# Kernel tuning notes

Measured on AMD Instinct MI355X. Metric: run time of the kernel, lower is better.

Reference implementation:

```python
import jax, jax.numpy as jnp
import numpy as np
import math

D_MODEL = 1024
N_HEADS = 16
D_HEAD = D_MODEL // N_HEADS


def setup_inputs() -> dict:
    key = jax.random.key(0)
    ks = jax.random.split(key, 5)
    B, T, C = 4, 2048, D_MODEL
    s = 1.0 / math.sqrt(C)
    return {
        "x": jax.random.normal(ks[0], (B, T, C), dtype=jnp.float32),
        "qkv_w": jax.random.normal(ks[1], (3 * C, C), dtype=jnp.float32) * s,
        "qkv_b": jnp.zeros((3 * C,), dtype=jnp.float32),
        "out_w": jax.random.normal(ks[2], (C, C), dtype=jnp.float32) * s,
        "out_b": jnp.zeros((C,), dtype=jnp.float32),
    }


def reference(x, qkv_w, qkv_b, out_w, out_b):
    B, T, C = x.shape
    H, Dh = N_HEADS, D_HEAD
    qkv = x @ qkv_w.T + qkv_b              # [B,T,3C] (torch Linear: x W^T + b)
    q, k, v = jnp.split(qkv, 3, axis=-1)
    # [B,T,C] -> [B,H,T,Dh]
    q = q.reshape(B, T, H, Dh).transpose(0, 2, 1, 3)
    k = k.reshape(B, T, H, Dh).transpose(0, 2, 1, 3)
    v = v.reshape(B, T, H, Dh).transpose(0, 2, 1, 3)
    att = jnp.einsum("bhqd,bhkd->bhqk", q, k) / math.sqrt(Dh)
    causal = jnp.tril(jnp.ones((T, T), dtype=bool))  # True = keep
    att = jnp.where(causal, att, -jnp.inf)
    att = jax.nn.softmax(att, axis=-1)
    y = jnp.einsum("bhqk,bhkd->bhqd", att, v)
    y = y.transpose(0, 2, 1, 3).reshape(B, T, C)
    return y @ out_w.T + out_b
```

## Files before the change

### kernel.cpp

```cpp
#include <hip/hip_runtime.h>

typedef __attribute__((ext_vector_type(4))) float f32x4;
typedef __attribute__((ext_vector_type(16))) float f32x16;
typedef __attribute__((ext_vector_type(8))) __bf16 bf16x8;
typedef __attribute__((ext_vector_type(4))) __bf16 bf16x4;
typedef __attribute__((ext_vector_type(2))) unsigned u32x2;

#define MFMA_B16(a,b,c) __builtin_amdgcn_mfma_f32_16x16x32_bf16((a),(b),(c),0,0,0)
#define MFMA32(a,b,c)  __builtin_amdgcn_mfma_f32_32x32x16_bf16((a),(b),(c),0,0,0)

static constexpr int T_LEN  = 2048;
static constexpr int C_DIM  = 1024;
static constexpr int H_NUM  = 16;
static constexpr int D_HEADc = 64;
static constexpr float Q_PRESCALE = 0.125f * 1.4426950408889634f;

__device__ __forceinline__ void async16(const void* g, void* l) {
  __builtin_amdgcn_global_load_lds(
      (const __attribute__((address_space(1))) unsigned int*)g,
      (__attribute__((address_space(3))) unsigned int*)l, 16, 0, 0);
}

__device__ __forceinline__ unsigned cvtpk(float lo, float hi) {
  unsigned r;
  asm("v_cvt_pk_bf16_f32 %0, %1, %2" : "=v"(r) : "v"(lo), "v"(hi));
  return r;
}

__global__ __launch_bounds__(256) void cvt3_kernel(const float* __restrict__ a, __bf16* __restrict__ da, int na,
                                                   const float* __restrict__ b, __bf16* __restrict__ db, int nb,
                                                   const float* __restrict__ c, __bf16* __restrict__ dc, int nc) {
  int i = blockIdx.x * 256 + threadIdx.x;
  const float* s;
  __bf16* d;
  long j;
  if (i < na) { s = a; d = da; j = i; }
  else if (i < na + nb) { s = b; d = db; j = i - na; }
  else if (i < na + nb + nc) { s = c; d = dc; j = i - na - nb; }
  else return;
  float4 f = reinterpret_cast<const float4*>(s)[j];
  bf16x4 o;
  o.x = (__bf16)f.x; o.y = (__bf16)f.y; o.z = (__bf16)f.z; o.w = (__bf16)f.w;
  reinterpret_cast<bf16x4*>(d)[j] = o;
}

__global__ __launch_bounds__(256) void gemm_qkv(const __bf16* __restrict__ A,
                                                const __bf16* __restrict__ W,
                                                const float* __restrict__ bias,
                                                __bf16* __restrict__ qb,
                                                __bf16* __restrict__ kb,
                                                __bf16* __restrict__ vb) {
  constexpr int K = 1024;
  __shared__ __bf16 As[128 * 64];
  __shared__ __bf16 Bs[128 * 64];
  const int tid = threadIdx.x;
  const int wid = tid >> 6, lane = tid & 63, l16 = lane & 15, lg = lane >> 4;
  const int r8 = lane >> 3, sl = lane & 7;
  const int r7 = l16 & 7;
  const int wm = wid >> 1, wn = wid & 1;
  const int m0 = blockIdx.x * 128, n0 = blockIdx.y * 128;

  f32x4 acc[4][4];
#pragma unroll
  for (int i = 0; i < 4; ++i)
#pragma unroll
    for (int j = 0; j < 4; ++j) acc[i][j] = f32x4{0.f, 0.f, 0.f, 0.f};

  for (int k0 = 0; k0 < K; k0 += 64) {
    __builtin_amdgcn_s_barrier();
#pragma unroll
    for (int it = 0; it < 4; ++it) {
      int chunk = it * 4 + wid;
      int row = chunk * 8 + r8;
      int scol = ((sl ^ (row & 7)) << 3);
      async16(A + (long)(m0 + row) * K + k0 + scol, &As[chunk * 512]);
      async16(W + (long)(n0 + row) * K + k0 + scol, &Bs[chunk * 512]);
    }
    asm volatile("s_waitcnt vmcnt(0)" ::: "memory");
    __builtin_amdgcn_s_barrier();
#pragma unroll
    for (int kt = 0; kt < 2; ++kt) {
      const int sw = ((((kt << 2) | lg) ^ r7) << 3);
      bf16x8 af[4], bfv[4];
#pragma unroll
      for (int mi = 0; mi < 4; ++mi)
        af[mi] = *reinterpret_cast<const bf16x8*>(&As[(wm * 64 + mi * 16 + l16) * 64 + sw]);
#pragma unroll
      for (int nt = 0; nt < 4; ++nt)
        bfv[nt] = *reinterpret_cast<const bf16x8*>(&Bs[(wn * 64 + nt * 16 + l16) * 64 + sw]);
#pragma unroll
      for (int mi = 0; mi < 4; ++mi)
#pragma unroll
        for (int nt = 0; nt < 4; ++nt)
          acc[mi][nt] = MFMA_B16(af[mi], bfv[nt], acc[mi][nt]);
    }
  }
#pragma unroll
  for (int mi = 0; mi < 4; ++mi)
#pragma unroll
    for (int nt = 0; nt < 4; ++nt)
#pragma unroll
      for (int r = 0; r < 4; ++r) {
        int m = m0 + wm * 64 + mi * 16 + lg * 4 + r;
        int n = n0 + wn * 64 + nt * 16 + l16;
        float val = acc[mi][nt][r] + bias[n];
        int which = n >> 10;
        int cc = n & 1023;
        int h = cc >> 6, d = cc & 63;
        long b = m >> 11;
        long t = m & 2047;
        if (which == 0) {
          qb[(((b * H_NUM + h) * T_LEN) + t) * D_HEADc + d] = (__bf16)(val * Q_PRESCALE);
        } else if (which == 1) {
          kb[(((b * H_NUM + h) * T_LEN) + t) * D_HEADc + d] = (__bf16)val;
        } else {
          vb[(((b * H_NUM + h) * D_HEADc) + d) * T_LEN + t] = (__bf16)val;
        }
      }
}

__global__ __launch_bounds__(256) void attn_kernel(const __bf16* __restrict__ q,
                                                   const __bf16* __restrict__ k,
                                                   const __bf16* __restrict__ vt,
                                                   __bf16* __restrict__ y) {
  __shared__ __bf16 Ks[2][64 * 64];
  __shared__ __bf16 Vs[2][64 * 64];
  const int tid = threadIdx.x;
  const int wid = tid >> 6, lane = tid & 63;
  const int l31 = lane & 31, hi = lane >> 5;
  const int r8 = lane >> 3, sl = lane & 7;
  const int r7 = l31 & 7;
  const int bid = blockIdx.x;
  const int pair = bid >> 6;
  const int bh = bid & 63;
  const __bf16* qg = q + (long)bh * T_LEN * D_HEADc;
  const __bf16* kg = k + (long)bh * T_LEN * D_HEADc;
  const __bf16* vg = vt + (long)bh * T_LEN * D_HEADc;
  const long bb = bh >> 4;
  const int h = bh & 15;

  union { unsigned short us[8]; bf16x8 v; } ones_u;
#pragma unroll
  for (int i = 0; i < 8; ++i) ones_u.us[i] = 0x3F80;
  const bf16x8 ones = ones_u.v;

  f32x16 z16;
#pragma unroll
  for (int r = 0; r < 16; ++r) z16[r] = 0.f;

  auto stage = [&](int buf, int t) {
    const int k0s = t * 64;
#pragma unroll
    for (int it = 0; it < 2; ++it) {
      int chunk = it * 4 + wid;
      int row = chunk * 8 + r8;
      int scol = ((sl ^ (row & 7)) << 3);
      async16(kg + (long)(k0s + row) * D_HEADc + scol, &Ks[buf][chunk * 512]);
      async16(vg + (long)row * T_LEN + k0s + scol, &Vs[buf][chunk * 512]);
    }
  };

  auto m3 = [](float a, float b, float c) { return fmaxf(fmaxf(a, b), c); };

  for (int ph = 0; ph < 2; ++ph) {
    const int qt = ph ? (15 - pair) : pair;
    const int q0 = qt * 128;
    const int qw = q0 + wid * 32;
    const int qglob = qw + l31;

    bf16x8 qf[4];
#pragma unroll
    for (int dt = 0; dt < 4; ++dt)
      qf[dt] = *reinterpret_cast<const bf16x8*>(qg + (long)qglob * D_HEADc + dt * 16 + hi * 8);

    f32x16 o[2];
    o[0] = z16; o[1] = z16;
    f32x16 lacc = z16;
    float m = -3e38f;

    const int ntiles = qt * 2 + 2;
    stage(0, 0);
    int cur = 0;
    for (int t = 0; t < ntiles; ++t) {
      if (t + 1 < ntiles) {
        stage(cur ^ 1, t + 1);
        asm volatile("s_waitcnt vmcnt(4)" ::: "memory");
      } else {
        asm volatile("s_waitcnt vmcnt(0)" ::: "memory");
      }
      __builtin_amdgcn_s_barrier();
      const int k0 = t * 64;
      if (k0 < qw + 32) {
        f32x16 s[2];
        __builtin_amdgcn_s_setprio(1);
        {
          const int swz = (hi ^ r7) << 3;
          bf16x8 kf0 = *reinterpret_cast<const bf16x8*>(&Ks[cur][l31 * 64 + swz]);
          bf16x8 kf1 = *reinterpret_cast<const bf16x8*>(&Ks[cur][(32 + l31) * 64 + swz]);
          s[0] = MFMA32(kf0, qf[0], z16);
          s[1] = MFMA32(kf1, qf[0], z16);
        }
#pragma unroll
        for (int dt = 1; dt < 4; ++dt) {
          const int swz = (((dt << 1) | hi) ^ r7) << 3;
          bf16x8 kf0 = *reinterpret_cast<const bf16x8*>(&Ks[cur][l31 * 64 + swz]);
          bf16x8 kf1 = *reinterpret_cast<const bf16x8*>(&Ks[cur][(32 + l31) * 64 + swz]);
          s[0] = MFMA32(kf0, qf[dt], s[0]);
          s[1] = MFMA32(kf1, qf[dt], s[1]);
        }
        __builtin_amdgcn_s_setprio(0);

        if (k0 + 63 > qw) {
#pragma unroll
          for (int r = 0; r < 16; ++r) {
            const int kb = (r & 3) + 8 * (r >> 2) + 4 * hi;
            if (k0 + kb > qglob) s[0][r] = -3e38f;
            if (k0 + 32 + kb > qglob) s[1][r] = -3e38f;
          }
        }

        float xv[11];
#pragma unroll
        for (int g = 0; g < 5; ++g) xv[g] = m3(s[0][3 * g], s[0][3 * g + 1], s[0][3 * g + 2]);
        xv[5] = m3(s[0][15], s[1][0], s[1][1]);
#pragma unroll
        for (int g = 0; g < 4; ++g) xv[6 + g] = m3(s[1][2 + 3 * g], s[1][3 + 3 * g], s[1][4 + 3 * g]);
        xv[10] = fmaxf(s[1][14], s[1][15]);
        float w0 = m3(xv[0], xv[1], xv[2]), w1 = m3(xv[3], xv[4], xv[5]);
        float w2 = m3(xv[6], xv[7], xv[8]), w3 = fmaxf(xv[9], xv[10]);
        float mx = fmaxf(m3(w0, w1, w2), w3);
        mx = fmaxf(mx, __shfl_xor(mx, 32));

        if (!__all(mx <= m + 8.f)) {
          const float mn = fmaxf(m, mx);
          const float al = exp2f(m - mn);
          m = mn;
          lacc[0] *= al;
#pragma unroll
          for (int di = 0; di < 2; ++di)
#pragma unroll
            for (int r = 0; r < 16; ++r) o[di][r] *= al;
        }
#pragma unroll
        for (int ki = 0; ki < 2; ++ki)
#pragma unroll
          for (int r = 0; r < 16; ++r) s[ki][r] = exp2f(s[ki][r] - m);

        unsigned pb[4][4];
#pragma unroll
        for (int ki = 0; ki < 2; ++ki) {
          unsigned d0 = cvtpk(s[ki][0], s[ki][1]),   d1 = cvtpk(s[ki][2], s[ki][3]);
          unsigned d2 = cvtpk(s[ki][4], s[ki][5]),   d3 = cvtpk(s[ki][6], s[ki][7]);
          unsigned d4 = cvtpk(s[ki][8], s[ki][9]),   d5 = cvtpk(s[ki][10], s[ki][11]);
          unsigned d6 = cvtpk(s[ki][12], s[ki][13]), d7 = cvtpk(s[ki][14], s[ki][15]);
          u32x2 a2 = __builtin_amdgcn_permlane32_swap(d0, d2, false, false);
          u32x2 b2 = __builtin_amdgcn_permlane32_swap(d1, d3, false, false);
          pb[ki * 2][0] = a2[0]; pb[ki * 2][1] = b2[0];
          pb[ki * 2][2] = a2[1]; pb[ki * 2][3] = b2[1];
          u32x2 c2 = __builtin_amdgcn_permlane32_swap(d4, d6, false, false);
          u32x2 e2 = __builtin_amdgcn_permlane32_swap(d5, d7, false, false);
          pb[ki * 2 + 1][0] = c2[0]; pb[ki * 2 + 1][1] = e2[0];
          pb[ki * 2 + 1][2] = c2[1]; pb[ki * 2 + 1][3] = e2[1];
        }

        __builtin_amdgcn_s_setprio(1);
#pragma unroll
        for (int kt = 0; kt < 4; ++kt) {
          union { unsigned u[4]; bf16x8 v; } pu;
#pragma unroll
          for (int w = 0; w < 4; ++w) pu.u[w] = pb[kt][w];
          const int swz = (((kt << 1) | hi) ^ r7) << 3;
          bf16x8 vf0 = *reinterpret_cast<const bf16x8*>(&Vs[cur][l31 * 64 + swz]);
          bf16x8 vf1 = *reinterpret_cast<const bf16x8*>(&Vs[cur][(32 + l31) * 64 + swz]);
          o[0] = MFMA32(vf0, pu.v, o[0]);
          o[1] = MFMA32(vf1, pu.v, o[1]);
          lacc = MFMA32(ones, pu.v, lacc);
        }
        __builtin_amdgcn_s_setprio(0);
      }
      __builtin_amdgcn_s_barrier();
      cur ^= 1;
    }

    const float inv = 1.f / lacc[0];
    const long row = bb * T_LEN + qglob;
#pragma unroll
    for (int di = 0; di < 2; ++di)
#pragma unroll
      for (int rr = 0; rr < 4; ++rr) {
        bf16x4 pk;
#pragma unroll
        for (int c = 0; c < 4; ++c) pk[c] = (__bf16)(o[di][rr * 4 + c] * inv);
        *reinterpret_cast<bf16x4*>(
            &y[row * C_DIM + h * D_HEADc + di * 32 + rr * 8 + hi * 4]) = pk;
      }
  }
}

__global__ __launch_bounds__(256) void gemm_proj(const __bf16* __restrict__ A,
                                                 const __bf16* __restrict__ W,
                                                 const float* __restrict__ bias,
                                                 float* __restrict__ out) {
  constexpr int K = 1024;
  __shared__ __bf16 As[128 * 64];
  __shared__ __bf16 Bs[128 * 64];
  const int tid = threadIdx.x;
  const int wid = tid >> 6, lane = tid & 63, l16 = lane & 15, lg = lane >> 4;
  const int r8 = lane >> 3, sl = lane & 7;
  const int r7 = l16 & 7;
  const int wm = wid >> 1, wn = wid & 1;
  const int m0 = blockIdx.x * 128, n0 = blockIdx.y * 128;

  f32x4 acc[4][4];
#pragma unroll
  for (int i = 0; i < 4; ++i)
#pragma unroll
    for (int j = 0; j < 4; ++j) acc[i][j] = f32x4{0.f, 0.f, 0.f, 0.f};

  for (int k0 = 0; k0 < K; k0 += 64) {
    __builtin_amdgcn_s_barrier();
#pragma unroll
    for (int it = 0; it < 4; ++it) {
      int chunk = it * 4 + wid;
      int row = chunk * 8 + r8;
      int scol = ((sl ^ (row & 7)) << 3);
      async16(A + (long)(m0 + row) * K + k0 + scol, &As[chunk * 512]);
      async16(W + (long)(n0 + row) * K + k0 + scol, &Bs[chunk * 512]);
    }
    asm volatile("s_waitcnt vmcnt(0)" ::: "memory");
    __builtin_amdgcn_s_barrier();
#pragma unroll
    for (int kt = 0; kt < 2; ++kt) {
      const int sw = ((((kt << 2) | lg) ^ r7) << 3);
      bf16x8 af[4], bfv[4];
#pragma unroll
      for (int mi = 0; mi < 4; ++mi)
        af[mi] = *reinterpret_cast<const bf16x8*>(&As[(wm * 64 + mi * 16 + l16) * 64 + sw]);
#pragma unroll
      for (int nt = 0; nt < 4; ++nt)
        bfv[nt] = *reinterpret_cast<const bf16x8*>(&Bs[(wn * 64 + nt * 16 + l16) * 64 + sw]);
#pragma unroll
      for (int mi = 0; mi < 4; ++mi)
#pragma unroll
        for (int nt = 0; nt < 4; ++nt)
          acc[mi][nt] = MFMA_B16(af[mi], bfv[nt], acc[mi][nt]);
    }
  }
#pragma unroll
  for (int mi = 0; mi < 4; ++mi)
#pragma unroll
    for (int nt = 0; nt < 4; ++nt)
#pragma unroll
      for (int r = 0; r < 4; ++r) {
        long m = m0 + wm * 64 + mi * 16 + lg * 4 + r;
        int n = n0 + wn * 64 + nt * 16 + l16;
        out[m * C_DIM + n] = acc[mi][nt][r] + bias[n];
      }
}

extern "C" void kernel_launch(void* const* d_in, const int* in_sizes, int n_in,
                              void* d_out, int out_size, void* d_ws, size_t ws_size,
                              hipStream_t stream) {
  const float* x     = (const float*)d_in[0];
  const float* qkv_w = (const float*)d_in[1];
  const float* qkv_b = (const float*)d_in[2];
  const float* out_w = (const float*)d_in[3];
  const float* out_b = (const float*)d_in[4];
  float* out = (float*)d_out;

  const long NX  = 8192L * 1024;
  const long NWQ = 3072L * 1024;
  const long NWO = 1024L * 1024;
  const size_t need = (size_t)(5 * NX + NWQ + NWO) * 2;
  if (ws_size < need) return;

  __bf16* xb   = (__bf16*)d_ws;
  __bf16* wqkv = xb + NX;
  __bf16* wout = wqkv + NWQ;
  __bf16* qb   = wout + NWO;
  __bf16* kb   = qb + NX;
  __bf16* vb   = kb + NX;
  __bf16* yb   = vb + NX;

  const int na = (int)(NX / 4), nb = (int)(NWQ / 4), nc = (int)(NWO / 4);
  cvt3_kernel<<<(na + nb + nc + 255) / 256, 256, 0, stream>>>(x, xb, na, qkv_w, wqkv, nb, out_w, wout, nc);

  gemm_qkv<<<dim3(64, 24), 256, 0, stream>>>(xb, wqkv, qkv_b, qb, kb, vb);
  attn_kernel<<<dim3(512), 256, 0, stream>>>(qb, kb, vb, yb);
  gemm_proj<<<dim3(64, 8), 256, 0, stream>>>(yb, wout, out_b, out);
}
```

Measured before the change: 199.3 us.

## Split attention KV loop across two wave groups with LDS merge

The attention kernel now runs 512 threads per block, one query tile per block, with two groups of four waves. Each group processes alternating 64-key tiles, and the groups' partial outputs and softmax stats are merged through LDS at the end. The old scheme, where each block paired two query tiles to balance causal work, is replaced by 1024 independent blocks ordered longest-first. This raises parallelism and shortens the per-block serial KV loop, at the cost of doubled LDS buffers, an extra merge step and possible idle waves on the odd last tile.

```diff
diff --git a/kernel.cpp b/kernel.cpp
--- a/kernel.cpp
+++ b/kernel.cpp
@@ -119,20 +119,25 @@
       }
 }
 
-__global__ __launch_bounds__(256) void attn_kernel(const __bf16* __restrict__ q,
-                                                   const __bf16* __restrict__ k,
-                                                   const __bf16* __restrict__ vt,
-                                                   __bf16* __restrict__ y) {
-  __shared__ __bf16 Ks[2][64 * 64];
-  __shared__ __bf16 Vs[2][64 * 64];
+__global__ __launch_bounds__(512, 4) void attn_kernel(const __bf16* __restrict__ q,
+                                                      const __bf16* __restrict__ k,
+                                                      const __bf16* __restrict__ vt,
+                                                      __bf16* __restrict__ y) {
+  __shared__ __bf16 Ks[2][2][64 * 64];
+  __shared__ __bf16 Vs[2][2][64 * 64];
   const int tid = threadIdx.x;
   const int wid = tid >> 6, lane = tid & 63;
   const int l31 = lane & 31, hi = lane >> 5;
   const int r8 = lane >> 3, sl = lane & 7;
   const int r7 = l31 & 7;
   const int bid = blockIdx.x;
-  const int pair = bid >> 6;
+  const int qt = 15 - (bid >> 6);
   const int bh = bid & 63;
+  const int grp = wid >> 2;
+  const int wq = wid & 3;
+  const int q0 = qt * 128;
+  const int qw = q0 + wq * 32;
+  const int qglob = qw + l31;
   const __bf16* qg = q + (long)bh * T_LEN * D_HEADc;
   const __bf16* kg = k + (long)bh * T_LEN * D_HEADc;
   const __bf16* vg = vt + (long)bh * T_LEN * D_HEADc;
@@ -148,141 +153,163 @@
 #pragma unroll
   for (int r = 0; r < 16; ++r) z16[r] = 0.f;
 
-  auto stage = [&](int buf, int t) {
-    const int k0s = t * 64;
-#pragma unroll
-    for (int it = 0; it < 2; ++it) {
-      int chunk = it * 4 + wid;
-      int row = chunk * 8 + r8;
+  bf16x8 qf[4];
+#pragma unroll
+  for (int dt = 0; dt < 4; ++dt)
+    qf[dt] = *reinterpret_cast<const bf16x8*>(qg + (long)qglob * D_HEADc + dt * 16 + hi * 8);
+
+  f32x16 o[2];
+  o[0] = z16; o[1] = z16;
+  f32x16 lacc = z16;
+  float m = -3e38f;
+
+  auto stage = [&](int buf, int i) {
+#pragma unroll
+    for (int it = 0; it < 4; ++it) {
+      int slot = it * 8 + wid;
+      int g = slot & 7;
+      int kind = slot >> 3;
+      int par = kind >> 1, isv = kind & 1;
+      int row = g * 8 + r8;
       int scol = ((sl ^ (row & 7)) << 3);
-      async16(kg + (long)(k0s + row) * D_HEADc + scol, &Ks[buf][chunk * 512]);
-      async16(vg + (long)row * T_LEN + k0s + scol, &Vs[buf][chunk * 512]);
+      int k0s = (2 * i + par) * 64;
+      if (!isv)
+        async16(kg + (long)(k0s + row) * D_HEADc + scol, &Ks[buf][par][g * 512]);
+      else
+        async16(vg + (long)row * T_LEN + k0s + scol, &Vs[buf][par][g * 512]);
     }
   };
 
   auto m3 = [](float a, float b, float c) { return fmaxf(fmaxf(a, b), c); };
 
-  for (int ph = 0; ph < 2; ++ph) {
-    const int qt = ph ? (15 - pair) : pair;
-    const int q0 = qt * 128;
-    const int qw = q0 + wid * 32;
-    const int qglob = qw + l31;
-
-    bf16x8 qf[4];
-#pragma unroll
-    for (int dt = 0; dt < 4; ++dt)
-      qf[dt] = *reinterpret_cast<const bf16x8*>(qg + (long)qglob * D_HEADc + dt * 16 + hi * 8);
-
-    f32x16 o[2];
-    o[0] = z16; o[1] = z16;
-    f32x16 lacc = z16;
-    float m = -3e38f;
-
-    const int ntiles = qt * 2 + 2;
-    stage(0, 0);
-    int cur = 0;
-    for (int t = 0; t < ntiles; ++t) {
-      if (t + 1 < ntiles) {
-        stage(cur ^ 1, t + 1);
-        asm volatile("s_waitcnt vmcnt(4)" ::: "memory");
-      } else {
-        asm volatile("s_waitcnt vmcnt(0)" ::: "memory");
-      }
-      __builtin_amdgcn_s_barrier();
-      const int k0 = t * 64;
-      if (k0 < qw + 32) {
-        f32x16 s[2];
-        __builtin_amdgcn_s_setprio(1);
-        {
-          const int swz = (hi ^ r7) << 3;
-          bf16x8 kf0 = *reinterpret_cast<const bf16x8*>(&Ks[cur][l31 * 64 + swz]);
-          bf16x8 kf1 = *reinterpret_cast<const bf16x8*>(&Ks[cur][(32 + l31) * 64 + swz]);
-          s[0] = MFMA32(kf0, qf[0], z16);
-          s[1] = MFMA32(kf1, qf[0], z16);
+  const int iters = qt + 1;
+  stage(0, 0);
+  int cur = 0;
+  for (int i = 0; i < iters; ++i) {
+    if (i + 1 < iters) {
+      stage(cur ^ 1, i + 1);
+      asm volatile("s_waitcnt vmcnt(4)" ::: "memory");
+    } else {
+      asm volatile("s_waitcnt vmcnt(0)" ::: "memory");
+    }
+    __builtin_amdgcn_s_barrier();
+    const int k0 = (2 * i + grp) * 64;
+    if (k0 < qw + 32) {
+      const __bf16* Kc = Ks[cur][grp];
+      const __bf16* Vc = Vs[cur][grp];
+      f32x16 s[2];
+      __builtin_amdgcn_s_setprio(1);
+      {
+        const int swz = (hi ^ r7) << 3;
+        bf16x8 kf0 = *reinterpret_cast<const bf16x8*>(&Kc[l31 * 64 + swz]);
+        bf16x8 kf1 = *reinterpret_cast<const bf16x8*>(&Kc[(32 + l31) * 64 + swz]);
+        s[0] = MFMA32(kf0, qf[0], z16);
+        s[1] = MFMA32(kf1, qf[0], z16);
+      }
+#pragma unroll
+      for (int dt = 1; dt < 4; ++dt) {
+        const int swz = (((dt << 1) | hi) ^ r7) << 3;
+        bf16x8 kf0 = *reinterpret_cast<const bf16x8*>(&Kc[l31 * 64 + swz]);
+        bf16x8 kf1 = *reinterpret_cast<const bf16x8*>(&Kc[(32 + l31) * 64 + swz]);
+        s[0] = MFMA32(kf0, qf[dt], s[0]);
+        s[1] = MFMA32(kf1, qf[dt], s[1]);
+      }
+      __builtin_amdgcn_s_setprio(0);
+
+      if (k0 + 63 > qw) {
+#pragma unroll
+        for (int r = 0; r < 16; ++r) {
+          const int kb = (r & 3) + 8 * (r >> 2) + 4 * hi;
+          if (k0 + kb > qglob) s[0][r] = -3e38f;
+          if (k0 + 32 + kb > qglob) s[1][r] = -3e38f;
         }
-#pragma unroll
-        for (int dt = 1; dt < 4; ++dt) {
-          const int swz = (((dt << 1) | hi) ^ r7) << 3;
-          bf16x8 kf0 = *reinterpret_cast<const bf16x8*>(&Ks[cur][l31 * 64 + swz]);
-          bf16x8 kf1 = *reinterpret_cast<const bf16x8*>(&Ks[cur][(32 + l31) * 64 + swz]);
-          s[0] = MFMA32(kf0, qf[dt], s[0]);
-          s[1] = MFMA32(kf1, qf[dt], s[1]);
-        }
-        __builtin_amdgcn_s_setprio(0);
-
-        if (k0 + 63 > qw) {
-#pragma unroll
-          for (int r = 0; r < 16; ++r) {
-            const int kb = (r & 3) + 8 * (r >> 2) + 4 * hi;
-            if (k0 + kb > qglob) s[0][r] = -3e38f;
-            if (k0 + 32 + kb > qglob) s[1][r] = -3e38f;
-          }
-        }
-
-        float xv[11];
-#pragma unroll
-        for (int g = 0; g < 5; ++g) xv[g] = m3(s[0][3 * g], s[0][3 * g + 1], s[0][3 * g + 2]);
-        xv[5] = m3(s[0][15], s[1][0], s[1][1]);
-#pragma unroll
-        for (int g = 0; g < 4; ++g) xv[6 + g] = m3(s[1][2 + 3 * g], s[1][3 + 3 * g], s[1][4 + 3 * g]);
-        xv[10] = fmaxf(s[1][14], s[1][15]);
-        float w0 = m3(xv[0], xv[1], xv[2]), w1 = m3(xv[3], xv[4], xv[5]);
-        float w2 = m3(xv[6], xv[7], xv[8]), w3 = fmaxf(xv[9], xv[10]);
-        float mx = fmaxf(m3(w0, w1, w2), w3);
-        mx = fmaxf(mx, __shfl_xor(mx, 32));
-
-        if (!__all(mx <= m + 8.f)) {
-          const float mn = fmaxf(m, mx);
-          const float al = exp2f(m - mn);
-          m = mn;
-          lacc[0] *= al;
-#pragma unroll
-          for (int di = 0; di < 2; ++di)
-#pragma unroll
-            for (int r = 0; r < 16; ++r) o[di][r] *= al;
-        }
-#pragma unroll
-        for (int ki = 0; ki < 2; ++ki)
-#pragma unroll
-          for (int r = 0; r < 16; ++r) s[ki][r] = exp2f(s[ki][r] - m);
-
-        unsigned pb[4][4];
-#pragma unroll
-        for (int ki = 0; ki < 2; ++ki) {
-          unsigned d0 = cvtpk(s[ki][0], s[ki][1]),   d1 = cvtpk(s[ki][2], s[ki][3]);
-          unsigned d2 = cvtpk(s[ki][4], s[ki][5]),   d3 = cvtpk(s[ki][6], s[ki][7]);
-          unsigned d4 = cvtpk(s[ki][8], s[ki][9]),   d5 = cvtpk(s[ki][10], s[ki][11]);
-          unsigned d6 = cvtpk(s[ki][12], s[ki][13]), d7 = cvtpk(s[ki][14], s[ki][15]);
-          u32x2 a2 = __builtin_amdgcn_permlane32_swap(d0, d2, false, false);
-          u32x2 b2 = __builtin_amdgcn_permlane32_swap(d1, d3, false, false);
-          pb[ki * 2][0] = a2[0]; pb[ki * 2][1] = b2[0];
-          pb[ki * 2][2] = a2[1]; pb[ki * 2][3] = b2[1];
-          u32x2 c2 = __builtin_amdgcn_permlane32_swap(d4, d6, false, false);
-          u32x2 e2 = __builtin_amdgcn_permlane32_swap(d5, d7, false, false);
-          pb[ki * 2 + 1][0] = c2[0]; pb[ki * 2 + 1][1] = e2[0];
-          pb[ki * 2 + 1][2] = c2[1]; pb[ki * 2 + 1][3] = e2[1];
-        }
-
-        __builtin_amdgcn_s_setprio(1);
-#pragma unroll
-        for (int kt = 0; kt < 4; ++kt) {
-          union { unsigned u[4]; bf16x8 v; } pu;
-#pragma unroll
-          for (int w = 0; w < 4; ++w) pu.u[w] = pb[kt][w];
-          const int swz = (((kt << 1) | hi) ^ r7) << 3;
-          bf16x8 vf0 = *reinterpret_cast<const bf16x8*>(&Vs[cur][l31 * 64 + swz]);
-          bf16x8 vf1 = *reinterpret_cast<const bf16x8*>(&Vs[cur][(32 + l31) * 64 + swz]);
-          o[0] = MFMA32(vf0, pu.v, o[0]);
-          o[1] = MFMA32(vf1, pu.v, o[1]);
-          lacc = MFMA32(ones, pu.v, lacc);
-        }
-        __builtin_amdgcn_s_setprio(0);
-      }
-      __builtin_amdgcn_s_barrier();
-      cur ^= 1;
-    }
-
-    const float inv = 1.f / lacc[0];
+      }
+
+      float xv[11];
+#pragma unroll
+      for (int g = 0; g < 5; ++g) xv[g] = m3(s[0][3 * g], s[0][3 * g + 1], s[0][3 * g + 2]);
+      xv[5] = m3(s[0][15], s[1][0], s[1][1]);
+#pragma unroll
+      for (int g = 0; g < 4; ++g) xv[6 + g] = m3(s[1][2 + 3 * g], s[1][3 + 3 * g], s[1][4 + 3 * g]);
+      xv[10] = fmaxf(s[1][14], s[1][15]);
+      float w0 = m3(xv[0], xv[1], xv[2]), w1 = m3(xv[3], xv[4], xv[5]);
+      float w2 = m3(xv[6], xv[7], xv[8]), w3 = fmaxf(xv[9], xv[10]);
+      float mx = fmaxf(m3(w0, w1, w2), w3);
+      mx = fmaxf(mx, __shfl_xor(mx, 32));
+
+      if (!__all(mx <= m + 8.f)) {
+        const float mn = fmaxf(m, mx);
+        const float al = exp2f(m - mn);
+        m = mn;
+        lacc[0] *= al;
+#pragma unroll
+        for (int di = 0; di < 2; ++di)
+#pragma unroll
+          for (int r = 0; r < 16; ++r) o[di][r] *= al;
+      }
+#pragma unroll
+      for (int ki = 0; ki < 2; ++ki)
+#pragma unroll
+        for (int r = 0; r < 16; ++r) s[ki][r] = exp2f(s[ki][r] - m);
+
+      unsigned pb[4][4];
+#pragma unroll
+      for (int ki = 0; ki < 2; ++ki) {
+        unsigned d0 = cvtpk(s[ki][0], s[ki][1]),   d1 = cvtpk(s[ki][2], s[ki][3]);
+        unsigned d2 = cvtpk(s[ki][4], s[ki][5]),   d3 = cvtpk(s[ki][6], s[ki][7]);
+        unsigned d4 = cvtpk(s[ki][8], s[ki][9]),   d5 = cvtpk(s[ki][10], s[ki][11]);
+        unsigned d6 = cvtpk(s[ki][12], s[ki][13]), d7 = cvtpk(s[ki][14], s[ki][15]);
+        u32x2 a2 = __builtin_amdgcn_permlane32_swap(d0, d2, false, false);
+        u32x2 b2 = __builtin_amdgcn_permlane32_swap(d1, d3, false, false);
+        pb[ki * 2][0] = a2[0]; pb[ki * 2][1] = b2[0];
+        pb[ki * 2][2] = a2[1]; pb[ki * 2][3] = b2[1];
+        u32x2 c2 = __builtin_amdgcn_permlane32_swap(d4, d6, false, false);
+        u32x2 e2 = __builtin_amdgcn_permlane32_swap(d5, d7, false, false);
+        pb[ki * 2 + 1][0] = c2[0]; pb[ki * 2 + 1][1] = e2[0];
+        pb[ki * 2 + 1][2] = c2[1]; pb[ki * 2 + 1][3] = e2[1];
+      }
+
+      __builtin_amdgcn_s_setprio(1);
+#pragma unroll
+      for (int kt = 0; kt < 4; ++kt) {
+        union { unsigned u[4]; bf16x8 v; } pu;
+#pragma unroll
+        for (int w = 0; w < 4; ++w) pu.u[w] = pb[kt][w];
+        const int swz = (((kt << 1) | hi) ^ r7) << 3;
+        bf16x8 vf0 = *reinterpret_cast<const bf16x8*>(&Vc[l31 * 64 + swz]);
+        bf16x8 vf1 = *reinterpret_cast<const bf16x8*>(&Vc[(32 + l31) * 64 + swz]);
+        o[0] = MFMA32(vf0, pu.v, o[0]);
+        o[1] = MFMA32(vf1, pu.v, o[1]);
+        lacc = MFMA32(ones, pu.v, lacc);
+      }
+      __builtin_amdgcn_s_setprio(0);
+    }
+    __builtin_amdgcn_s_barrier();
+    cur ^= 1;
+  }
+
+  float* ob  = (float*)&Ks[0][0][0];
+  float* mlb = (float*)&Vs[0][0][0];
+  if (grp == 1) {
+#pragma unroll
+    for (int di = 0; di < 2; ++di)
+#pragma unroll
+      for (int r = 0; r < 16; ++r) {
+        const int kb = (r & 3) + 8 * (r >> 2) + 4 * hi;
+        ob[wq * 2048 + (di * 32 + kb) * 32 + l31] = o[di][r];
+      }
+    if (hi == 0) {
+      mlb[wq * 32 + l31] = m;
+      mlb[128 + wq * 32 + l31] = lacc[0];
+    }
+  }
+  __syncthreads();
+  if (grp == 0) {
+    const float m1 = mlb[wq * 32 + l31];
+    const float l1 = mlb[128 + wq * 32 + l31];
+    const float mn = fmaxf(m, m1);
+    const float al0 = exp2f(m - mn), al1 = exp2f(m1 - mn);
+    const float inv = 1.f / (lacc[0] * al0 + l1 * al1);
     const long row = bb * T_LEN + qglob;
 #pragma unroll
     for (int di = 0; di < 2; ++di)
@@ -290,7 +317,12 @@
       for (int rr = 0; rr < 4; ++rr) {
         bf16x4 pk;
 #pragma unroll
-        for (int c = 0; c < 4; ++c) pk[c] = (__bf16)(o[di][rr * 4 + c] * inv);
+        for (int c = 0; c < 4; ++c) {
+          const int r = rr * 4 + c;
+          const int kb = rr * 8 + hi * 4 + c;
+          float val = o[di][r] * al0 + ob[wq * 2048 + (di * 32 + kb) * 32 + l31] * al1;
+          pk[c] = (__bf16)(val * inv);
+        }
         *reinterpret_cast<bf16x4*>(
             &y[row * C_DIM + h * D_HEADc + di * 32 + rr * 8 + hi * 4]) = pk;
       }
@@ -386,6 +418,6 @@
   cvt3_kernel<<<(na + nb + nc + 255) / 256, 256, 0, stream>>>(x, xb, na, qkv_w, wqkv, nb, out_w, wout, nc);
 
   gemm_qkv<<<dim3(64, 24), 256, 0, stream>>>(xb, wqkv, qkv_b, qb, kb, vb);
-  attn_kernel<<<dim3(512), 256, 0, stream>>>(qb, kb, vb, yb);
+  attn_kernel<<<dim3(1024), 512, 0, stream>>>(qb, kb, vb, yb);
   gemm_proj<<<dim3(64, 8), 256, 0, stream>>>(yb, wout, out_b, out);
 }
```

Measured after the change: 188.5 us. -5.4%, faster.
